# Optimization experiments

Measured on AMD Instinct MI355X. Metric: run time of the kernel, lower is better.

Reference implementation:

```python
import jax, jax.numpy as jnp
import numpy as np

# norse LIFParameters / LIParameters defaults
DT = 1e-3
TAU_SYN_INV = 200.0   # 1/5e-3
TAU_MEM_INV = 100.0   # 1/1e-2
V_TH = 1.0
V_LEAK = 0.0
V_RESET = 0.0
ALPHA = 100.0         # super-spike surrogate slope
SEQ = 10              # ConstantCurrentLIFEncoder(10)
SCALE = 50.0

@jax.custom_vjp
def superspike(x):
    # forward: Heaviside; backward: SuperSpike surrogate 1/(alpha|x|+1)^2
    return (x > 0).astype(x.dtype)

def _ss_fwd(x):
    return superspike(x), x

def _ss_bwd(x, g):
    return (g / (ALPHA * jnp.abs(x) + 1.0) ** 2,)

superspike.defvjp(_ss_fwd, _ss_bwd)

def constant_current_lif_encode(current):
    # current: (B, S) constant input current; returns spikes (SEQ, B, S)
    def step(v, _):
        v = v + DT * TAU_MEM_INV * ((V_LEAK - v) + current)
        z = superspike(v - V_TH)
        v = v - z * (v - V_RESET)
        return v, z
    _, spikes = jax.lax.scan(step, jnp.zeros_like(current), None, length=SEQ)
    return spikes

def setup_inputs() -> dict:
    key = jax.random.key(0)
    k1, k2, k3, k4 = jax.random.split(key, 4)
    B, S, H, A = 2048, 2048, 256, 16
    x = jax.random.normal(k1, (B, S), dtype=jnp.float32)
    w_in = jax.random.normal(k2, (H, 2 * S), dtype=jnp.float32) * np.float32(np.sqrt(2.0 / H))
    w_rec = jax.random.normal(k3, (H, H), dtype=jnp.float32) * np.float32(np.sqrt(2.0 / H))
    w_rec = w_rec * (1.0 - jnp.eye(H, dtype=jnp.float32))  # no autapses
    w_out = jax.random.normal(k4, (A, H), dtype=jnp.float32) * np.float32(np.sqrt(2.0 / H))
    return {"x": x, "w_in": w_in, "w_rec": w_rec, "w_out": w_out}

def reference(x, w_in, w_rec, w_out):
    # PPOSNN.pi(x): encode, LIF recurrent scan, LI readout, max over time, softmax
    enc = jnp.concatenate(
        [constant_current_lif_encode(jax.nn.relu(SCALE * x)),
         constant_current_lif_encode(jax.nn.relu(-SCALE * x))],
        axis=2,
    )  # (SEQ, B, 2S)
    B = x.shape[0]
    H = w_rec.shape[0]
    A = w_out.shape[0]
    z0 = jnp.zeros((B, H), x.dtype)
    v0 = jnp.zeros((B, H), x.dtype)
    i0 = jnp.zeros((B, H), x.dtype)
    vo0 = jnp.zeros((B, A), x.dtype)
    io0 = jnp.zeros((B, A), x.dtype)

    def step(carry, inp):
        z, v, i, vo, io = carry
        # LIFRecurrentCell (norse lif_step)
        v_dec = v + DT * TAU_MEM_INV * ((V_LEAK - v) + i)
        i_dec = i * (1.0 - DT * TAU_SYN_INV)
        z_new = superspike(v_dec - V_TH)
        v_new = (1.0 - z_new) * v_dec + z_new * V_RESET
        i_new = i_dec + inp @ w_in.T + z @ w_rec.T
        # LILinearCell (norse li_step) on z_new
        vo_new = vo + DT * TAU_MEM_INV * ((V_LEAK - vo) + io)
        io_new = io * (1.0 - DT * TAU_SYN_INV) + z_new @ w_out.T
        return (z_new, v_new, i_new, vo_new, io_new), vo_new

    _, voltages = jax.lax.scan(step, (z0, v0, i0, vo0, io0), enc)  # (SEQ, B, A)
    m = jnp.max(voltages, axis=0)
    m = jnp.where(jnp.isnan(m), jnp.zeros_like(m), m)
    return jax.nn.softmax(m, axis=1)
```

## Files before the change

### kernel.cpp

```cpp
#include <hip/hip_runtime.h>
#include <stdint.h>
#include <stddef.h>

typedef __attribute__((ext_vector_type(8))) short short8;
typedef __attribute__((ext_vector_type(4))) float f32x4;
typedef __attribute__((ext_vector_type(4))) uint32_t u32x4;

#define GLD_LDS16(gsrc, ldst)                                                   \
    __builtin_amdgcn_global_load_lds(                                           \
        (const __attribute__((address_space(1))) uint32_t*)(const void*)(gsrc), \
        (__attribute__((address_space(3))) uint32_t*)(void*)(ldst), 16, 0, 0)

static __device__ __forceinline__ uint16_t bf16_rne(float f) {
    uint32_t u = __float_as_uint(f);
    uint32_t r = u + 0x7FFFu + ((u >> 16) & 1u);
    return (uint16_t)(r >> 16);
}
static __device__ __forceinline__ float bf16_f(uint16_t h) {
    return __uint_as_float(((uint32_t)h) << 16);
}

#define OFF_MASKS 0u
#define SZ_MASKS  (2048u * 4096u * 2u)
#define OFF_WIN   (OFF_MASKS + SZ_MASKS)
#define SZ_WIN1   (256u * 4096u * 2u)
#define OFF_WREC  (OFF_WIN + 3u * SZ_WIN1)
#define SZ_WREC1  (256u * 256u * 2u)
#define OFF_WOUT  (OFF_WREC + 2u * SZ_WREC1)
#define SZ_WOUT1  (16u * 256u * 2u)
#define OFF_IIN   (OFF_WOUT + 2u * SZ_WOUT1)

__global__ __launch_bounds__(256) void k_prep(const float* __restrict__ x,
                                              uint16_t* __restrict__ masks) {
    int g = blockIdx.x * 256 + threadIdx.x;
    int b = g >> 11, s = g & 2047;
    float q = 50.0f * x[g];
    float c = fabsf(q);
    float v = 0.0f;
    uint32_t m = 0u;
    #pragma unroll
    for (int t = 0; t < 10; ++t) {
        v = v + 0.1f * ((0.0f - v) + c);
        if (v > 1.0f) { m |= (1u << t); v = 0.0f; }
    }
    masks[(size_t)b * 4096 + s]        = (q > 0.0f) ? (uint16_t)m : (uint16_t)0;
    masks[(size_t)b * 4096 + 2048 + s] = (q < 0.0f) ? (uint16_t)m : (uint16_t)0;
}

__global__ __launch_bounds__(256) void k_wsplit(const float* __restrict__ win,
                                                const float* __restrict__ wrec,
                                                const float* __restrict__ wout,
                                                uint16_t* __restrict__ win_s,
                                                uint16_t* __restrict__ wrec_s,
                                                uint16_t* __restrict__ wout_s) {
    int g = blockIdx.x * 256 + threadIdx.x;
    if (g < 1048576) {
        float w = win[g];
        uint16_t h = bf16_rne(w);
        float r1 = w - bf16_f(h);
        uint16_t md = bf16_rne(r1);
        float r2 = r1 - bf16_f(md);
        win_s[g]            = h;
        win_s[1048576 + g]  = md;
        win_s[2097152 + g]  = bf16_rne(r2);
    } else if (g < 1114112) {
        int i = g - 1048576;
        float w = wrec[i];
        uint16_t h = bf16_rne(w);
        float r1 = w - bf16_f(h);
        wrec_s[i]         = h;
        wrec_s[65536 + i] = bf16_rne(r1);
    } else if (g < 1118208) {
        int i = g - 1114112;
        float w = wout[i];
        uint16_t h = bf16_rne(w);
        float r1 = w - bf16_f(h);
        wout_s[i]        = h;
        wout_s[4096 + i] = bf16_rne(r1);
    }
}

__global__ __launch_bounds__(256) void k_gemm(const uint16_t* __restrict__ masks,
                                              const uint16_t* __restrict__ wsp,
                                              float* __restrict__ iin) {
    __shared__ uint16_t Abuf[2][80 * 64];
    __shared__ uint16_t Bbuf[3][128 * 64];
    const int tid = threadIdx.x;
    const int lane = tid & 63;
    const int wid = tid >> 6;
    const int l15 = lane & 15;
    const int lq = lane >> 4;
    const int Mtile = blockIdx.x >> 1;
    const int Ntile = blockIdx.x & 1;
    const int M0 = Mtile * 80;

    const int c0 = tid;
    const int c1 = tid + 256;

    uint32_t mq[2][8];

    auto loadMasks = [&](int kk) {
        {
            int r = c0 >> 2, k16 = (c0 & 3) << 4;
            uint32_t m = (uint32_t)(M0 + r);
            uint32_t b = (m * 52429u) >> 19;
            const u32x4* mp = (const u32x4*)(masks + (size_t)b * 4096 + (size_t)(kk * 64 + k16));
            u32x4 q0 = mp[0], q1 = mp[1];
            #pragma unroll
            for (int j = 0; j < 4; ++j) { mq[0][j] = q0[j]; mq[0][4 + j] = q1[j]; }
        }
        if (c1 < 320) {
            int r = c1 >> 2, k16 = (c1 & 3) << 4;
            uint32_t m = (uint32_t)(M0 + r);
            uint32_t b = (m * 52429u) >> 19;
            const u32x4* mp = (const u32x4*)(masks + (size_t)b * 4096 + (size_t)(kk * 64 + k16));
            u32x4 q0 = mp[0], q1 = mp[1];
            #pragma unroll
            for (int j = 0; j < 4; ++j) { mq[1][j] = q0[j]; mq[1][4 + j] = q1[j]; }
        }
    };

    auto expandWrite = [&](int ab) {
        #pragma unroll
        for (int ci = 0; ci < 2; ++ci) {
            int c = (ci == 0) ? c0 : c1;
            if (c >= 320) break;
            int r = c >> 2, k16 = (c & 3) << 4;
            uint32_t m = (uint32_t)(M0 + r);
            uint32_t b = (m * 52429u) >> 19;
            uint32_t t = m - b * 10u;
            u32x4 o0, o1;
            #pragma unroll
            for (int j = 0; j < 4; ++j) {
                uint32_t x0 = mq[ci][j] >> t;
                uint32_t x1 = mq[ci][4 + j] >> t;
                o0[j] = (x0 & 1u) * 0x3F80u + (x0 & 0x10000u) * 0x3F80u;
                o1[j] = (x1 & 1u) * 0x3F80u + (x1 & 0x10000u) * 0x3F80u;
            }
            uint32_t swz = (uint32_t)((r & 7) << 4);
            uint32_t base = (uint32_t)(r * 128 + (k16 << 1));
            char* dst = (char*)Abuf[ab];
            *(u32x4*)(dst + (base ^ swz)) = o0;
            *(u32x4*)(dst + ((base + 16u) ^ swz)) = o1;
        }
    };

    auto stageB = [&](int kk, int s, uint16_t* bufp) {
        const char* src = (const char*)wsp + (size_t)s * 2097152u;
        char* dst = (char*)bufp;
        #pragma unroll
        for (int p = 0; p < 4; ++p) {
            int c = (p << 8) + tid;
            int n = c >> 3;
            uint32_t off = (uint32_t)((c & 7) << 4);
            uint32_t so = (uint32_t)(Ntile * 128 + n) * 8192u + (uint32_t)(kk << 7)
                        + (off ^ (uint32_t)((n & 7) << 4));
            GLD_LDS16(src + so, dst + (size_t)c * 16u);
        }
    };

    short8 af[5][2];
    f32x4 acc[5][2];
    #pragma unroll
    for (int mt = 0; mt < 5; ++mt)
        #pragma unroll
        for (int nt = 0; nt < 2; ++nt)
            #pragma unroll
            for (int q = 0; q < 4; ++q) acc[mt][nt][q] = 0.0f;

    auto readA = [&](int ab) {
        #pragma unroll
        for (int mt = 0; mt < 5; ++mt)
            #pragma unroll
            for (int kt = 0; kt < 2; ++kt) {
                int row = mt * 16 + l15;
                uint32_t byte = (uint32_t)(row * 128)
                              + ((uint32_t)((kt << 6) + (lq << 4)) ^ (uint32_t)((row & 7) << 4));
                af[mt][kt] = *(const short8*)((const char*)Abuf[ab] + byte);
            }
    };
    auto mfmaPhase = [&](const uint16_t* Bpp) {
        short8 bf[2][2];
        #pragma unroll
        for (int nt = 0; nt < 2; ++nt)
            #pragma unroll
            for (int kt = 0; kt < 2; ++kt) {
                int n = (wid << 5) + nt * 16 + l15;
                uint32_t byte = (uint32_t)(n * 128)
                              + ((uint32_t)((kt << 6) + (lq << 4)) ^ (uint32_t)((n & 7) << 4));
                bf[nt][kt] = *(const short8*)((const char*)Bpp + byte);
            }
        __builtin_amdgcn_s_setprio(1);
        #pragma unroll
        for (int kt = 0; kt < 2; ++kt)
            #pragma unroll
            for (int mt = 0; mt < 5; ++mt)
                #pragma unroll
                for (int nt = 0; nt < 2; ++nt)
                    acc[mt][nt] = __builtin_amdgcn_mfma_f32_16x16x32_bf16(
                        af[mt][kt], bf[nt][kt], acc[mt][nt], 0, 0, 0);
        __builtin_amdgcn_s_setprio(0);
    };

    loadMasks(0);
    expandWrite(0);
    stageB(0, 0, Bbuf[0]);

    #pragma unroll 1
    for (int kk = 0; kk < 64; ++kk) {
        const int ab = kk & 1;
        const bool more = (kk < 63);
        if (more) loadMasks(kk + 1);
        __builtin_amdgcn_sched_barrier(0);
        stageB(kk, 1, Bbuf[1]);
        if (more) asm volatile("s_waitcnt vmcnt(6) lgkmcnt(0)" ::: "memory");
        else      asm volatile("s_waitcnt vmcnt(4) lgkmcnt(0)" ::: "memory");
        __builtin_amdgcn_s_barrier();
        __builtin_amdgcn_sched_barrier(0);
        readA(ab);
        mfmaPhase(Bbuf[0]);
        if (more) expandWrite(ab ^ 1);
        __builtin_amdgcn_sched_barrier(0);
        stageB(kk, 2, Bbuf[2]);
        asm volatile("s_waitcnt vmcnt(4) lgkmcnt(0)" ::: "memory");
        __builtin_amdgcn_s_barrier();
        __builtin_amdgcn_sched_barrier(0);
        mfmaPhase(Bbuf[1]);
        if (more) {
            stageB(kk + 1, 0, Bbuf[0]);
            asm volatile("s_waitcnt vmcnt(4) lgkmcnt(0)" ::: "memory");
        } else {
            asm volatile("s_waitcnt vmcnt(0) lgkmcnt(0)" ::: "memory");
        }
        __builtin_amdgcn_s_barrier();
        __builtin_amdgcn_sched_barrier(0);
        mfmaPhase(Bbuf[2]);
    }

    #pragma unroll
    for (int mt = 0; mt < 5; ++mt)
        #pragma unroll
        for (int nt = 0; nt < 2; ++nt)
            #pragma unroll
            for (int i = 0; i < 4; ++i) {
                int gm = M0 + mt * 16 + (lq << 2) + i;
                int h = Ntile * 128 + (wid << 5) + nt * 16 + l15;
                iin[(size_t)gm * 256 + h] = acc[mt][nt][i];
            }
}

__global__ __launch_bounds__(256) void k_scan(const float* __restrict__ iin,
                                              const uint16_t* __restrict__ wrec_s,
                                              const uint16_t* __restrict__ wout_s,
                                              float* __restrict__ out) {
    __shared__ uint16_t Z[2][16 * 256];
    __shared__ uint16_t Bb[3][256 * 64];
    __shared__ uint16_t WO[2][16 * 256];
    const int tid = threadIdx.x;
    const int lane = tid & 63;
    const int wid = tid >> 6;
    const int l15 = lane & 15;
    const int lq = lane >> 4;
    const int b0 = blockIdx.x << 4;

    #pragma unroll
    for (int s = 0; s < 2; ++s) {
        #pragma unroll
        for (int p = 0; p < 2; ++p) {
            int c = (p << 8) + tid;
            int n = c >> 5;
            uint32_t off = (uint32_t)((c & 31) << 4);
            u32x4 v = *(const u32x4*)((const char*)(wout_s + (size_t)s * 4096) + (size_t)n * 512 + off);
            *(u32x4*)((char*)WO[s] + (uint32_t)(n * 512) + (off ^ (uint32_t)((n & 7) << 4))) = v;
        }
    }
    #pragma unroll
    for (int p = 0; p < 8; ++p) ((uint32_t*)Z[0])[(p << 8) + tid] = 0u;

    auto stageBrec = [&](int g, int db) {
        int jj = g & 7;
        int sp = jj >> 2;
        int ks = jj & 3;
        const char* src = (const char*)(wrec_s + (size_t)sp * 65536);
        char* dst = (char*)Bb[db];
        #pragma unroll
        for (int p = 0; p < 8; ++p) {
            int c = (p << 8) + tid;
            int n = c >> 3;
            uint32_t off = (uint32_t)((c & 7) << 4);
            uint32_t so = (uint32_t)(n * 512) + (uint32_t)(ks << 7) + (off ^ (uint32_t)((n & 7) << 4));
            GLD_LDS16(src + so, dst + (size_t)c * 16);
        }
    };
    stageBrec(0, 0);
    asm volatile("s_waitcnt lgkmcnt(0)" ::: "memory");
    __builtin_amdgcn_s_barrier();

    float vst[4][4], ist[4][4];
    #pragma unroll
    for (int nf = 0; nf < 4; ++nf)
        #pragma unroll
        for (int r = 0; r < 4; ++r) { vst[nf][r] = 0.0f; ist[nf][r] = 0.0f; }
    float io_[4] = {0.f, 0.f, 0.f, 0.f};
    float vo_[4] = {0.f, 0.f, 0.f, 0.f};
    float mm[4] = {-1e30f, -1e30f, -1e30f, -1e30f};

    int cur = 0;
    #pragma unroll 1
    for (int t = 0; t < 10; ++t) {
        const int pp = t & 1;
        f32x4 acc[4];
        #pragma unroll
        for (int nf = 0; nf < 4; ++nf) {
            #pragma unroll
            for (int r = 0; r < 4; ++r) {
                float vv = vst[nf][r];
                float ii = ist[nf][r];
                float vd = vv + 0.1f * ((0.0f - vv) + ii);
                bool z = (vd > 1.0f);
                vst[nf][r] = z ? 0.0f : vd;
                int brow = (lq << 2) + r;
                int h = (wid << 6) + (nf << 4) + l15;
                uint32_t byte = (uint32_t)(brow * 512)
                              + ((uint32_t)(h << 1) ^ (uint32_t)((brow & 7) << 4));
                *(uint16_t*)((char*)Z[pp ^ 1] + byte) = z ? (uint16_t)0x3F80u : (uint16_t)0u;
                float I = iin[(size_t)((b0 + brow) * 10 + t) * 256 + h];
                acc[nf][r] = 0.8f * ii + I;
            }
        }
        for (int j = 0; j < 8; ++j) {
            int g = (t << 3) + j;
            int nxt = (cur == 2) ? 0 : cur + 1;
            if (g + 1 < 80) {
                stageBrec(g + 1, nxt);
                asm volatile("s_waitcnt vmcnt(8) lgkmcnt(0)" ::: "memory");
            } else {
                asm volatile("s_waitcnt vmcnt(0) lgkmcnt(0)" ::: "memory");
            }
            __builtin_amdgcn_s_barrier();
            __builtin_amdgcn_sched_barrier(0);
            int ks = j & 3;
            short8 az[2];
            #pragma unroll
            for (int kt = 0; kt < 2; ++kt) {
                int kb = (ks << 7) + (kt << 6) + (lq << 4);
                uint32_t byte = (uint32_t)(l15 * 512)
                              + ((uint32_t)kb ^ (uint32_t)((l15 & 7) << 4));
                az[kt] = *(const short8*)((const char*)Z[pp] + byte);
            }
            const char* Bp = (const char*)Bb[cur];
            __builtin_amdgcn_s_setprio(1);
            #pragma unroll
            for (int nf = 0; nf < 4; ++nf) {
                int n = (wid << 6) + (nf << 4) + l15;
                #pragma unroll
                for (int kt = 0; kt < 2; ++kt) {
                    uint32_t byte = (uint32_t)(n * 128)
                                  + ((uint32_t)((kt << 6) + (lq << 4)) ^ (uint32_t)((n & 7) << 4));
                    short8 bw = *(const short8*)(Bp + byte);
                    acc[nf] = __builtin_amdgcn_mfma_f32_16x16x32_bf16(az[kt], bw, acc[nf], 0, 0, 0);
                }
            }
            __builtin_amdgcn_s_setprio(0);
            cur = nxt;
        }
        #pragma unroll
        for (int nf = 0; nf < 4; ++nf)
            #pragma unroll
            for (int r = 0; r < 4; ++r) ist[nf][r] = acc[nf][r];

        if (wid == 0) {
            f32x4 aio;
            #pragma unroll
            for (int r = 0; r < 4; ++r) aio[r] = 0.8f * io_[r];
            #pragma unroll
            for (int s = 0; s < 2; ++s) {
                #pragma unroll
                for (int kc = 0; kc < 8; ++kc) {
                    int kb = (kc << 6) + (lq << 4);
                    uint32_t byte = (uint32_t)(l15 * 512)
                                  + ((uint32_t)kb ^ (uint32_t)((l15 & 7) << 4));
                    short8 azn = *(const short8*)((const char*)Z[pp ^ 1] + byte);
                    short8 bwo = *(const short8*)((const char*)WO[s] + byte);
                    aio = __builtin_amdgcn_mfma_f32_16x16x32_bf16(azn, bwo, aio, 0, 0, 0);
                }
            }
            #pragma unroll
            for (int r = 0; r < 4; ++r) {
                float von = vo_[r] + 0.1f * ((0.0f - vo_[r]) + io_[r]);
                io_[r] = aio[r];
                vo_[r] = von;
                mm[r] = fmaxf(mm[r], von);
            }
        }
        __builtin_amdgcn_s_barrier();
    }

    if (wid == 0) {
        #pragma unroll
        for (int r = 0; r < 4; ++r) {
            float mv = mm[r];
            if (mv != mv) mv = 0.0f;
            float mx = mv;
            #pragma unroll
            for (int d = 1; d < 16; d <<= 1) mx = fmaxf(mx, __shfl_xor(mx, d));
            float e = __expf(mv - mx);
            float ss = e;
            #pragma unroll
            for (int d = 1; d < 16; d <<= 1) ss += __shfl_xor(ss, d);
            out[(size_t)(b0 + (lq << 2) + r) * 16 + l15] = e / ss;
        }
    }
}

extern "C" void kernel_launch(void* const* d_in, const int* in_sizes, int n_in,
                              void* d_out, int out_size, void* d_ws, size_t ws_size,
                              hipStream_t stream) {
    (void)in_sizes; (void)n_in; (void)out_size; (void)ws_size;
    const float* x     = (const float*)d_in[0];
    const float* w_in  = (const float*)d_in[1];
    const float* w_rec = (const float*)d_in[2];
    const float* w_out = (const float*)d_in[3];
    float* out = (float*)d_out;
    char* ws = (char*)d_ws;
    uint16_t* masks  = (uint16_t*)(ws + OFF_MASKS);
    uint16_t* win_s  = (uint16_t*)(ws + OFF_WIN);
    uint16_t* wrec_s = (uint16_t*)(ws + OFF_WREC);
    uint16_t* wout_s = (uint16_t*)(ws + OFF_WOUT);
    float* iin = (float*)(ws + OFF_IIN);

    k_prep  <<<dim3(16384), dim3(256), 0, stream>>>(x, masks);
    k_wsplit<<<dim3(4368),  dim3(256), 0, stream>>>(w_in, w_rec, w_out, win_s, wrec_s, wout_s);
    k_gemm  <<<dim3(512),   dim3(256), 0, stream>>>(masks, win_s, iin);
    k_scan  <<<dim3(128),   dim3(256), 0, stream>>>(iin, wrec_s, wout_s, out);
}
```

Baseline: 245.7 us.

## Use 32x32 MFMA with register-expanded masks in GEMM and halve scan batch per block

The input GEMM drops the LDS staging buffer for the A operand. Spike masks are now expanded directly into registers and fed to 32x32x16 bf16 MFMAs over 64-row M tiles, with 640 blocks and a 3-blocks-per-CU launch bound. The recurrent scan kernel now handles 8 batch rows per block across 256 blocks and stages the weights in 128-wide K chunks, double-buffered. It uses a single Z buffer guarded by extra barriers. The aim is to cut LDS traffic and raise parallelism, at the cost of half of each scan MFMA being wasted on padded rows and more synchronisation.

```diff
diff --git a/kernel.cpp b/kernel.cpp
--- a/kernel.cpp
+++ b/kernel.cpp
@@ -4,6 +4,7 @@
 
 typedef __attribute__((ext_vector_type(8))) short short8;
 typedef __attribute__((ext_vector_type(4))) float f32x4;
+typedef __attribute__((ext_vector_type(16))) float f32x16;
 typedef __attribute__((ext_vector_type(4))) uint32_t u32x4;
 
 #define GLD_LDS16(gsrc, ldst)                                                   \
@@ -80,69 +81,53 @@
     }
 }
 
-__global__ __launch_bounds__(256) void k_gemm(const uint16_t* __restrict__ masks,
-                                              const uint16_t* __restrict__ wsp,
-                                              float* __restrict__ iin) {
-    __shared__ uint16_t Abuf[2][80 * 64];
+__global__ __launch_bounds__(256, 3) void k_gemm(const uint16_t* __restrict__ masks,
+                                                 const uint16_t* __restrict__ wsp,
+                                                 float* __restrict__ iin) {
     __shared__ uint16_t Bbuf[3][128 * 64];
     const int tid = threadIdx.x;
     const int lane = tid & 63;
     const int wid = tid >> 6;
-    const int l15 = lane & 15;
-    const int lq = lane >> 4;
+    const int l31 = lane & 31;
+    const int hi  = lane >> 5;
     const int Mtile = blockIdx.x >> 1;
     const int Ntile = blockIdx.x & 1;
-    const int M0 = Mtile * 80;
-
-    const int c0 = tid;
-    const int c1 = tid + 256;
-
-    uint32_t mq[2][8];
-
+    const int M0 = Mtile * 64;
+
+    uint32_t bb[2], tt[2];
+    #pragma unroll
+    for (int mf = 0; mf < 2; ++mf) {
+        uint32_t m = (uint32_t)(M0 + mf * 32 + l31);
+        uint32_t b = (m * 52429u) >> 19;
+        bb[mf] = b;
+        tt[mf] = m - b * 10u;
+    }
+
+    u32x4 mq[2][4];
     auto loadMasks = [&](int kk) {
-        {
-            int r = c0 >> 2, k16 = (c0 & 3) << 4;
-            uint32_t m = (uint32_t)(M0 + r);
-            uint32_t b = (m * 52429u) >> 19;
-            const u32x4* mp = (const u32x4*)(masks + (size_t)b * 4096 + (size_t)(kk * 64 + k16));
-            u32x4 q0 = mp[0], q1 = mp[1];
-            #pragma unroll
-            for (int j = 0; j < 4; ++j) { mq[0][j] = q0[j]; mq[0][4 + j] = q1[j]; }
-        }
-        if (c1 < 320) {
-            int r = c1 >> 2, k16 = (c1 & 3) << 4;
-            uint32_t m = (uint32_t)(M0 + r);
-            uint32_t b = (m * 52429u) >> 19;
-            const u32x4* mp = (const u32x4*)(masks + (size_t)b * 4096 + (size_t)(kk * 64 + k16));
-            u32x4 q0 = mp[0], q1 = mp[1];
-            #pragma unroll
-            for (int j = 0; j < 4; ++j) { mq[1][j] = q0[j]; mq[1][4 + j] = q1[j]; }
+        #pragma unroll
+        for (int mf = 0; mf < 2; ++mf) {
+            const uint16_t* mp = masks + (size_t)bb[mf] * 4096 + (size_t)(kk * 64 + hi * 8);
+            #pragma unroll
+            for (int ks = 0; ks < 4; ++ks)
+                mq[mf][ks] = *(const u32x4*)(mp + ks * 16);
         }
     };
 
-    auto expandWrite = [&](int ab) {
-        #pragma unroll
-        for (int ci = 0; ci < 2; ++ci) {
-            int c = (ci == 0) ? c0 : c1;
-            if (c >= 320) break;
-            int r = c >> 2, k16 = (c & 3) << 4;
-            uint32_t m = (uint32_t)(M0 + r);
-            uint32_t b = (m * 52429u) >> 19;
-            uint32_t t = m - b * 10u;
-            u32x4 o0, o1;
-            #pragma unroll
-            for (int j = 0; j < 4; ++j) {
-                uint32_t x0 = mq[ci][j] >> t;
-                uint32_t x1 = mq[ci][4 + j] >> t;
-                o0[j] = (x0 & 1u) * 0x3F80u + (x0 & 0x10000u) * 0x3F80u;
-                o1[j] = (x1 & 1u) * 0x3F80u + (x1 & 0x10000u) * 0x3F80u;
-            }
-            uint32_t swz = (uint32_t)((r & 7) << 4);
-            uint32_t base = (uint32_t)(r * 128 + (k16 << 1));
-            char* dst = (char*)Abuf[ab];
-            *(u32x4*)(dst + (base ^ swz)) = o0;
-            *(u32x4*)(dst + ((base + 16u) ^ swz)) = o1;
-        }
+    short8 af[2][4];
+    auto expand = [&]() {
+        #pragma unroll
+        for (int mf = 0; mf < 2; ++mf)
+            #pragma unroll
+            for (int ks = 0; ks < 4; ++ks) {
+                u32x4 o;
+                #pragma unroll
+                for (int w = 0; w < 4; ++w) {
+                    uint32_t x = mq[mf][ks][w] >> tt[mf];
+                    o[w] = (x & 0x10001u) * 0x3F80u;
+                }
+                af[mf][ks] = *(short8*)&o;
+            }
     };
 
     auto stageB = [&](int kk, int s, uint16_t* bufp) {
@@ -159,109 +144,108 @@
         }
     };
 
-    short8 af[5][2];
-    f32x4 acc[5][2];
-    #pragma unroll
-    for (int mt = 0; mt < 5; ++mt)
-        #pragma unroll
-        for (int nt = 0; nt < 2; ++nt)
-            #pragma unroll
-            for (int q = 0; q < 4; ++q) acc[mt][nt][q] = 0.0f;
-
-    auto readA = [&](int ab) {
-        #pragma unroll
-        for (int mt = 0; mt < 5; ++mt)
-            #pragma unroll
-            for (int kt = 0; kt < 2; ++kt) {
-                int row = mt * 16 + l15;
-                uint32_t byte = (uint32_t)(row * 128)
-                              + ((uint32_t)((kt << 6) + (lq << 4)) ^ (uint32_t)((row & 7) << 4));
-                af[mt][kt] = *(const short8*)((const char*)Abuf[ab] + byte);
-            }
-    };
-    auto mfmaPhase = [&](const uint16_t* Bpp) {
-        short8 bf[2][2];
-        #pragma unroll
-        for (int nt = 0; nt < 2; ++nt)
-            #pragma unroll
-            for (int kt = 0; kt < 2; ++kt) {
-                int n = (wid << 5) + nt * 16 + l15;
-                uint32_t byte = (uint32_t)(n * 128)
-                              + ((uint32_t)((kt << 6) + (lq << 4)) ^ (uint32_t)((n & 7) << 4));
-                bf[nt][kt] = *(const short8*)((const char*)Bpp + byte);
-            }
+    f32x16 acc[2];
+    #pragma unroll
+    for (int mf = 0; mf < 2; ++mf)
+        #pragma unroll
+        for (int q = 0; q < 16; ++q) acc[mf][q] = 0.0f;
+
+    auto mfmaPhase = [&](const uint16_t* Bp) {
+        short8 bf[4];
+        const int n = (wid << 5) + l31;
+        #pragma unroll
+        for (int ks = 0; ks < 4; ++ks) {
+            uint32_t byte = (uint32_t)(n * 128)
+                          + ((uint32_t)((ks << 5) + (hi << 4)) ^ (uint32_t)((n & 7) << 4));
+            bf[ks] = *(const short8*)((const char*)Bp + byte);
+        }
         __builtin_amdgcn_s_setprio(1);
         #pragma unroll
-        for (int kt = 0; kt < 2; ++kt)
-            #pragma unroll
-            for (int mt = 0; mt < 5; ++mt)
-                #pragma unroll
-                for (int nt = 0; nt < 2; ++nt)
-                    acc[mt][nt] = __builtin_amdgcn_mfma_f32_16x16x32_bf16(
-                        af[mt][kt], bf[nt][kt], acc[mt][nt], 0, 0, 0);
+        for (int ks = 0; ks < 4; ++ks)
+            #pragma unroll
+            for (int mf = 0; mf < 2; ++mf)
+                acc[mf] = __builtin_amdgcn_mfma_f32_32x32x16_bf16(
+                    af[mf][ks], bf[ks], acc[mf], 0, 0, 0);
         __builtin_amdgcn_s_setprio(0);
     };
 
     loadMasks(0);
-    expandWrite(0);
     stageB(0, 0, Bbuf[0]);
+    asm volatile("s_waitcnt vmcnt(4)" ::: "memory");
+    expand();
 
     #pragma unroll 1
     for (int kk = 0; kk < 64; ++kk) {
-        const int ab = kk & 1;
         const bool more = (kk < 63);
-        if (more) loadMasks(kk + 1);
-        __builtin_amdgcn_sched_barrier(0);
         stageB(kk, 1, Bbuf[1]);
-        if (more) asm volatile("s_waitcnt vmcnt(6) lgkmcnt(0)" ::: "memory");
-        else      asm volatile("s_waitcnt vmcnt(4) lgkmcnt(0)" ::: "memory");
+        asm volatile("s_waitcnt vmcnt(4)" ::: "memory");
         __builtin_amdgcn_s_barrier();
         __builtin_amdgcn_sched_barrier(0);
-        readA(ab);
         mfmaPhase(Bbuf[0]);
-        if (more) expandWrite(ab ^ 1);
-        __builtin_amdgcn_sched_barrier(0);
         stageB(kk, 2, Bbuf[2]);
-        asm volatile("s_waitcnt vmcnt(4) lgkmcnt(0)" ::: "memory");
+        if (more) {
+            loadMasks(kk + 1);
+            asm volatile("s_waitcnt vmcnt(12)" ::: "memory");
+        } else {
+            asm volatile("s_waitcnt vmcnt(4)" ::: "memory");
+        }
         __builtin_amdgcn_s_barrier();
         __builtin_amdgcn_sched_barrier(0);
         mfmaPhase(Bbuf[1]);
         if (more) {
             stageB(kk + 1, 0, Bbuf[0]);
-            asm volatile("s_waitcnt vmcnt(4) lgkmcnt(0)" ::: "memory");
+            asm volatile("s_waitcnt vmcnt(4)" ::: "memory");
         } else {
-            asm volatile("s_waitcnt vmcnt(0) lgkmcnt(0)" ::: "memory");
+            asm volatile("s_waitcnt vmcnt(0)" ::: "memory");
         }
         __builtin_amdgcn_s_barrier();
         __builtin_amdgcn_sched_barrier(0);
         mfmaPhase(Bbuf[2]);
-    }
-
-    #pragma unroll
-    for (int mt = 0; mt < 5; ++mt)
-        #pragma unroll
-        for (int nt = 0; nt < 2; ++nt)
-            #pragma unroll
-            for (int i = 0; i < 4; ++i) {
-                int gm = M0 + mt * 16 + (lq << 2) + i;
-                int h = Ntile * 128 + (wid << 5) + nt * 16 + l15;
-                iin[(size_t)gm * 256 + h] = acc[mt][nt][i];
-            }
+        if (more) expand();
+    }
+
+    #pragma unroll
+    for (int mf = 0; mf < 2; ++mf)
+        #pragma unroll
+        for (int r = 0; r < 16; ++r) {
+            int row = (r & 3) + ((r >> 2) << 3) + (hi << 2);
+            int gm = M0 + mf * 32 + row;
+            int h = Ntile * 128 + (wid << 5) + l31;
+            iin[(size_t)gm * 256 + h] = acc[mf][r];
+        }
 }
 
 __global__ __launch_bounds__(256) void k_scan(const float* __restrict__ iin,
                                               const uint16_t* __restrict__ wrec_s,
                                               const uint16_t* __restrict__ wout_s,
                                               float* __restrict__ out) {
-    __shared__ uint16_t Z[2][16 * 256];
-    __shared__ uint16_t Bb[3][256 * 64];
+    __shared__ uint16_t Bb[2][256 * 128];
+    __shared__ uint16_t Zb[16 * 256];
     __shared__ uint16_t WO[2][16 * 256];
     const int tid = threadIdx.x;
     const int lane = tid & 63;
     const int wid = tid >> 6;
     const int l15 = lane & 15;
     const int lq = lane >> 4;
-    const int b0 = blockIdx.x << 4;
+    const int b0 = blockIdx.x << 3;
+
+    auto stageBrec = [&](int g, int db) {
+        int sp = (g >> 1) & 1;
+        int kh = g & 1;
+        const char* src = (const char*)wrec_s + (size_t)sp * 131072u;
+        char* dst = (char*)Bb[db];
+        #pragma unroll
+        for (int p = 0; p < 16; ++p) {
+            int c = (p << 8) + tid;
+            int n = c >> 4;
+            uint32_t x0 = (uint32_t)((c & 15) << 4);
+            uint32_t so = (uint32_t)(n * 512) + (uint32_t)(kh << 8)
+                        + (x0 ^ (uint32_t)((n & 7) << 4));
+            GLD_LDS16(src + so, dst + (size_t)c * 16);
+        }
+    };
+
+    stageBrec(0, 0);
 
     #pragma unroll
     for (int s = 0; s < 2; ++s) {
@@ -275,24 +259,8 @@
         }
     }
     #pragma unroll
-    for (int p = 0; p < 8; ++p) ((uint32_t*)Z[0])[(p << 8) + tid] = 0u;
-
-    auto stageBrec = [&](int g, int db) {
-        int jj = g & 7;
-        int sp = jj >> 2;
-        int ks = jj & 3;
-        const char* src = (const char*)(wrec_s + (size_t)sp * 65536);
-        char* dst = (char*)Bb[db];
-        #pragma unroll
-        for (int p = 0; p < 8; ++p) {
-            int c = (p << 8) + tid;
-            int n = c >> 3;
-            uint32_t off = (uint32_t)((c & 7) << 4);
-            uint32_t so = (uint32_t)(n * 512) + (uint32_t)(ks << 7) + (off ^ (uint32_t)((n & 7) << 4));
-            GLD_LDS16(src + so, dst + (size_t)c * 16);
-        }
-    };
-    stageBrec(0, 0);
+    for (int p = 0; p < 8; ++p) ((uint32_t*)Zb)[(p << 8) + tid] = 0u;
+
     asm volatile("s_waitcnt lgkmcnt(0)" ::: "memory");
     __builtin_amdgcn_s_barrier();
 
@@ -305,69 +273,85 @@
     float vo_[4] = {0.f, 0.f, 0.f, 0.f};
     float mm[4] = {-1e30f, -1e30f, -1e30f, -1e30f};
 
-    int cur = 0;
     #pragma unroll 1
     for (int t = 0; t < 10; ++t) {
-        const int pp = t & 1;
         f32x4 acc[4];
+        uint32_t zb[4];
         #pragma unroll
         for (int nf = 0; nf < 4; ++nf) {
+            zb[nf] = 0u;
             #pragma unroll
             for (int r = 0; r < 4; ++r) {
+                int brow = (lq << 2) + r;
                 float vv = vst[nf][r];
                 float ii = ist[nf][r];
                 float vd = vv + 0.1f * ((0.0f - vv) + ii);
                 bool z = (vd > 1.0f);
                 vst[nf][r] = z ? 0.0f : vd;
-                int brow = (lq << 2) + r;
+                if (z) zb[nf] |= (1u << r);
                 int h = (wid << 6) + (nf << 4) + l15;
-                uint32_t byte = (uint32_t)(brow * 512)
-                              + ((uint32_t)(h << 1) ^ (uint32_t)((brow & 7) << 4));
-                *(uint16_t*)((char*)Z[pp ^ 1] + byte) = z ? (uint16_t)0x3F80u : (uint16_t)0u;
-                float I = iin[(size_t)((b0 + brow) * 10 + t) * 256 + h];
+                int rowc = brow < 8 ? brow : 7;
+                float I = iin[(size_t)((b0 + rowc) * 10 + t) * 256 + h];
+                I = (brow < 8) ? I : 0.0f;
                 acc[nf][r] = 0.8f * ii + I;
             }
         }
-        for (int j = 0; j < 8; ++j) {
-            int g = (t << 3) + j;
-            int nxt = (cur == 2) ? 0 : cur + 1;
-            if (g + 1 < 80) {
-                stageBrec(g + 1, nxt);
-                asm volatile("s_waitcnt vmcnt(8) lgkmcnt(0)" ::: "memory");
+        for (int j = 0; j < 4; ++j) {
+            int g = (t << 2) + j;
+            int kh = g & 1;
+            __builtin_amdgcn_s_barrier();
+            if (g + 1 < 40) {
+                stageBrec(g + 1, (g + 1) & 1);
+                asm volatile("s_waitcnt vmcnt(16)" ::: "memory");
             } else {
-                asm volatile("s_waitcnt vmcnt(0) lgkmcnt(0)" ::: "memory");
+                asm volatile("s_waitcnt vmcnt(0)" ::: "memory");
             }
             __builtin_amdgcn_s_barrier();
             __builtin_amdgcn_sched_barrier(0);
-            int ks = j & 3;
-            short8 az[2];
-            #pragma unroll
-            for (int kt = 0; kt < 2; ++kt) {
-                int kb = (ks << 7) + (kt << 6) + (lq << 4);
+            short8 az[4];
+            #pragma unroll
+            for (int kt = 0; kt < 4; ++kt) {
                 uint32_t byte = (uint32_t)(l15 * 512)
-                              + ((uint32_t)kb ^ (uint32_t)((l15 & 7) << 4));
-                az[kt] = *(const short8*)((const char*)Z[pp] + byte);
-            }
-            const char* Bp = (const char*)Bb[cur];
+                              + ((uint32_t)((kh << 8) + (kt << 6) + (lq << 4))
+                                 ^ (uint32_t)((l15 & 7) << 4));
+                az[kt] = *(const short8*)((const char*)Zb + byte);
+            }
+            const char* Bp = (const char*)Bb[g & 1];
             __builtin_amdgcn_s_setprio(1);
             #pragma unroll
             for (int nf = 0; nf < 4; ++nf) {
                 int n = (wid << 6) + (nf << 4) + l15;
                 #pragma unroll
-                for (int kt = 0; kt < 2; ++kt) {
-                    uint32_t byte = (uint32_t)(n * 128)
+                for (int kt = 0; kt < 4; ++kt) {
+                    uint32_t byte = (uint32_t)(n * 256)
                                   + ((uint32_t)((kt << 6) + (lq << 4)) ^ (uint32_t)((n & 7) << 4));
                     short8 bw = *(const short8*)(Bp + byte);
                     acc[nf] = __builtin_amdgcn_mfma_f32_16x16x32_bf16(az[kt], bw, acc[nf], 0, 0, 0);
                 }
             }
             __builtin_amdgcn_s_setprio(0);
-            cur = nxt;
         }
         #pragma unroll
         for (int nf = 0; nf < 4; ++nf)
             #pragma unroll
             for (int r = 0; r < 4; ++r) ist[nf][r] = acc[nf][r];
+
+        __builtin_amdgcn_s_barrier();
+        #pragma unroll
+        for (int nf = 0; nf < 4; ++nf)
+            #pragma unroll
+            for (int r = 0; r < 4; ++r) {
+                int brow = (lq << 2) + r;
+                if (brow < 8) {
+                    int h = (wid << 6) + (nf << 4) + l15;
+                    uint32_t byte = (uint32_t)(brow * 512)
+                                  + ((uint32_t)(h << 1) ^ (uint32_t)((brow & 7) << 4));
+                    *(uint16_t*)((char*)Zb + byte) =
+                        ((zb[nf] >> r) & 1u) ? (uint16_t)0x3F80u : (uint16_t)0u;
+                }
+            }
+        asm volatile("s_waitcnt lgkmcnt(0)" ::: "memory");
+        __builtin_amdgcn_s_barrier();
 
         if (wid == 0) {
             f32x4 aio;
@@ -380,7 +364,7 @@
                     int kb = (kc << 6) + (lq << 4);
                     uint32_t byte = (uint32_t)(l15 * 512)
                                   + ((uint32_t)kb ^ (uint32_t)((l15 & 7) << 4));
-                    short8 azn = *(const short8*)((const char*)Z[pp ^ 1] + byte);
+                    short8 azn = *(const short8*)((const char*)Zb + byte);
                     short8 bwo = *(const short8*)((const char*)WO[s] + byte);
                     aio = __builtin_amdgcn_mfma_f32_16x16x32_bf16(azn, bwo, aio, 0, 0, 0);
                 }
@@ -393,10 +377,9 @@
                 mm[r] = fmaxf(mm[r], von);
             }
         }
-        __builtin_amdgcn_s_barrier();
-    }
-
-    if (wid == 0) {
+    }
+
+    if (wid == 0 && lq < 2) {
         #pragma unroll
         for (int r = 0; r < 4; ++r) {
             float mv = mm[r];
@@ -431,6 +414,6 @@
 
     k_prep  <<<dim3(16384), dim3(256), 0, stream>>>(x, masks);
     k_wsplit<<<dim3(4368),  dim3(256), 0, stream>>>(w_in, w_rec, w_out, win_s, wrec_s, wout_s);
-    k_gemm  <<<dim3(512),   dim3(256), 0, stream>>>(masks, win_s, iin);
-    k_scan  <<<dim3(128),   dim3(256), 0, stream>>>(iin, wrec_s, wout_s, out);
-}
+    k_gemm  <<<dim3(640),   dim3(256), 0, stream>>>(masks, win_s, iin);
+    k_scan  <<<dim3(256),   dim3(256), 0, stream>>>(iin, wrec_s, wout_s, out);
+}
```

New measurement: 303.4 us. +23.5%, slower.
